# Optimization experiments

Measured on AMD Instinct MI355X. Metric: run time of the kernel, lower is better.

Reference implementation:

```python
import jax, jax.numpy as jnp
import numpy as np

H = 1024      # hidden_size
NH = 16       # attention heads
DH = H // NH  # head dim
B, S = 4, 2048
EPS = 1e-12


def setup_inputs() -> dict:
    key = jax.random.key(0)
    ks = jax.random.split(key, 9)
    sc = 1.0 / np.sqrt(H)
    inp = {
        "input_tensor": jax.random.normal(ks[0], (B, S, H), dtype=jnp.float32),
        "Wq": jax.random.normal(ks[1], (H, H), dtype=jnp.float32) * sc,
        "bq": jnp.zeros((H,), jnp.float32),
        "Wk": jax.random.normal(ks[2], (H, H), dtype=jnp.float32) * sc,
        "bk": jnp.zeros((H,), jnp.float32),
        "Wv": jax.random.normal(ks[3], (H, H), dtype=jnp.float32) * sc,
        "bv": jnp.zeros((H,), jnp.float32),
        "Wo": jax.random.normal(ks[4], (H, H), dtype=jnp.float32) * sc,
        "bo": jnp.zeros((H,), jnp.float32),
        "gamma": jnp.ones((H,), jnp.float32),
        "beta": jnp.zeros((H,), jnp.float32),
    }
    return inp


def _heads(x):
    # [B,S,H] -> [B,NH,S,DH]
    b, s, _ = x.shape
    return x.reshape(b, s, NH, DH).transpose(0, 2, 1, 3)


def reference(input_tensor, Wq, bq, Wk, bk, Wv, bv, Wo, bo, gamma, beta):
    q = _heads(input_tensor @ Wq.T + bq)
    k = _heads(input_tensor @ Wk.T + bk)
    v = _heads(input_tensor @ Wv.T + bv)
    scores = jnp.einsum("bhqd,bhkd->bhqk", q, k) / jnp.sqrt(jnp.float32(DH))
    probs = jax.nn.softmax(scores, axis=-1)  # dropout p=0 -> identity
    ctx = jnp.einsum("bhqk,bhkd->bhqd", probs, v)
    ctx = ctx.transpose(0, 2, 1, 3).reshape(input_tensor.shape)  # [B,S,H]
    h = ctx @ Wo.T + bo
    x = h + input_tensor
    u = jnp.mean(x, axis=-1, keepdims=True)
    s2 = jnp.mean((x - u) ** 2, axis=-1, keepdims=True)
    xn = (x - u) / jnp.sqrt(s2 + EPS)
    return gamma * xn + beta
```

## Files before the change

kernel.cpp:

```cpp
#include <hip/hip_runtime.h>
#include <math.h>

#define H   1024
#define NH  16
#define DH  64
#define BB  4
#define SS  2048
#define M_ROWS (BB*SS)
#define EPS 1e-12f
#define QSCALE 0.18033688011112042f

typedef __attribute__((ext_vector_type(4))) float f32x4;
typedef __attribute__((ext_vector_type(8))) short bf16x8;
typedef const __attribute__((address_space(1))) void* as1cvp;
typedef __attribute__((address_space(3))) void*       as3vp;
typedef const __attribute__((address_space(1))) ushort* as1u;
typedef __attribute__((address_space(3))) ushort*       as3u;

__device__ __forceinline__ unsigned short f2bf(float f) {
    union { float f; unsigned u; } x; x.f = f;
    unsigned r = x.u + 0x7fffu + ((x.u >> 16) & 1u);
    return (unsigned short)(r >> 16);
}
__device__ __forceinline__ unsigned pk2bf(float lo, float hi) {
    return __builtin_amdgcn_perm(__float_as_uint(hi), __float_as_uint(lo), 0x07060302u);
}

__global__ __launch_bounds__(256)
void cvt_all(const float4* __restrict__ x,
             const float4* __restrict__ wq, const float4* __restrict__ wk,
             const float4* __restrict__ wv, const float4* __restrict__ wo,
             ushort4* __restrict__ xb, ushort4* __restrict__ wqb,
             ushort4* __restrict__ wkb, ushort4* __restrict__ wvb,
             ushort4* __restrict__ wob)
{
    int id = blockIdx.x * 256 + threadIdx.x;
    const float4* src; ushort4* dst; int off;
    if (id < 2097152) { src = x; dst = xb; off = id; }
    else {
        int t = id - 2097152, wsel = t >> 18;
        off = t & 262143;
        src = wsel == 0 ? wq : wsel == 1 ? wk : wsel == 2 ? wv : wo;
        dst = wsel == 0 ? wqb : wsel == 1 ? wkb : wsel == 2 ? wvb : wob;
    }
    float4 v = src[off];
    ushort4 o; o.x = f2bf(v.x); o.y = f2bf(v.y); o.z = f2bf(v.z); o.w = f2bf(v.w);
    dst[off] = o;
}

#define GL(gsrc, ldst) __builtin_amdgcn_global_load_lds((as1cvp)(gsrc), (as3vp)(ldst), 16, 0, 0)
#define STAGE_T(ofs, kt)                                                        \
    GL(gA + aOff  + (kt) * 64,      lds + (ofs) + w512);                        \
    GL(gA + aOff  + (kt) * 64 + 32, lds + (ofs) + 4096 + w512);                 \
    GL(gB + bOff0 + (kt) * 64,      lds + (ofs) + 8192 + w1024);                \
    GL(gB + bOff0 + (kt) * 64 + 32, lds + (ofs) + 16384 + w1024);               \
    GL(gB + bOff1 + (kt) * 64,      lds + (ofs) + 8192 + w1024 + 512);          \
    GL(gB + bOff1 + (kt) * 64 + 32, lds + (ofs) + 16384 + w1024 + 512);

__device__ __forceinline__ void gemm_core_256(const ushort* __restrict__ A,
                                              const ushort* __restrict__ Wt,
                                              ushort* ldsP,
                                              int row0, int col0, int K,
                                              f32x4 (&acc)[4][4])
{
    const int tid = threadIdx.x, lane = tid & 63, w = tid >> 6;
    const int wr = w >> 2, wc = w & 3, l15 = lane & 15, quad = lane >> 4;
    const int qsw = (quad ^ ((l15 >> 1) & 3)) * 8;

    const int sc = (lane & 3) ^ ((lane >> 3) & 3);

    const as1u gA = (as1u)A;
    const as1u gB = (as1u)Wt;
    as3u lds = (as3u)ldsP;

    const size_t aOff  = (size_t)(row0 + w * 16 + (lane >> 2)) * K + sc * 8;
    const size_t bOff0 = (size_t)(col0 + w * 32 + (lane >> 2)) * K + sc * 8;
    const size_t bOff1 = (size_t)(col0 + w * 32 + 16 + (lane >> 2)) * K + sc * 8;
    const int w512 = w * 512, w1024 = w * 1024;

    const int NT = K >> 6;
    STAGE_T(0, 0);
    STAGE_T(24576, 1);

    int cur = 0;
    for (int t = 0; t < NT; ++t) {
        if (t + 1 < NT) asm volatile("s_waitcnt vmcnt(6)" ::: "memory");
        else            asm volatile("s_waitcnt vmcnt(0)" ::: "memory");
        __builtin_amdgcn_s_barrier();

        int nxt2 = cur + 49152; if (nxt2 >= 73728) nxt2 -= 73728;
        if (t + 2 < NT) { STAGE_T(nxt2, t + 2); }

        const ushort* base = ldsP + cur;
        #pragma unroll
        for (int h = 0; h < 2; ++h) {
            const ushort* Ah = base + h * 4096;
            const ushort* Bh = base + 8192 + h * 8192;
            bf16x8 af[4], bfr[4];
            #pragma unroll
            for (int rt = 0; rt < 4; ++rt)
                af[rt] = *(const bf16x8*)&Ah[(wr * 64 + rt * 16 + l15) * 32 + qsw];
            #pragma unroll
            for (int ct = 0; ct < 4; ++ct)
                bfr[ct] = *(const bf16x8*)&Bh[(wc * 64 + ct * 16 + l15) * 32 + qsw];
            #pragma unroll
            for (int rt = 0; rt < 4; ++rt)
                #pragma unroll
                for (int ct = 0; ct < 4; ++ct)
                    acc[rt][ct] = __builtin_amdgcn_mfma_f32_16x16x32_bf16(af[rt], bfr[ct], acc[rt][ct], 0, 0, 0);
        }
        cur += 24576; if (cur == 73728) cur = 0;
    }
}

__global__ __launch_bounds__(512, 2)
void qkv_gemm(const ushort* __restrict__ xb,
              const ushort* __restrict__ Wqb, const ushort* __restrict__ Wkb,
              const ushort* __restrict__ Wvb,
              const float* __restrict__ bq, const float* __restrict__ bk,
              const float* __restrict__ bv,
              ushort* __restrict__ Qb, ushort* __restrict__ Kb, ushort* __restrict__ Vt)
{
    __shared__ __align__(16) ushort Ls[3 * 24576];
    const int lin = blockIdx.x;
    const int swz = (lin & 7) * 96 + (lin >> 3);
    const int z   = swz >> 8;
    const int rem = swz & 255;
    const int row0 = (rem >> 2) * 128;
    const int col0 = (rem & 3) * 256;

    const ushort* Wt  = z == 0 ? Wqb : z == 1 ? Wkb : Wvb;
    const float* bias = z == 0 ? bq  : z == 1 ? bk  : bv;

    f32x4 acc[4][4];
    #pragma unroll
    for (int i = 0; i < 4; ++i)
        #pragma unroll
        for (int j = 0; j < 4; ++j)
            acc[i][j] = (f32x4){0.f, 0.f, 0.f, 0.f};

    gemm_core_256(xb, Wt, Ls, row0, col0, H, acc);

    const int tid = threadIdx.x, lane = tid & 63, w = tid >> 6;
    const int wr = w >> 2, wc = w & 3, l15 = lane & 15, quad = lane >> 4;

    #pragma unroll
    for (int rt = 0; rt < 4; ++rt) {
        const int r0g = row0 + wr * 64 + rt * 16 + quad * 4;
        #pragma unroll
        for (int ct = 0; ct < 4; ++ct) {
            const int c = col0 + wc * 64 + ct * 16 + l15;
            const float bs = bias[c];
            if (z == 0) {
                #pragma unroll
                for (int i = 0; i < 4; ++i)
                    Qb[(size_t)(r0g + i) * H + c] = f2bf((acc[rt][ct][i] + bs) * QSCALE);
            } else if (z == 1) {
                #pragma unroll
                for (int i = 0; i < 4; ++i)
                    Kb[(size_t)(r0g + i) * H + c] = f2bf(acc[rt][ct][i] + bs);
            } else {
                const int bb = r0g >> 11, s0 = r0g & 2047;
                const int hh = c >> 6, dd = c & 63;
                ushort4 o;
                o.x = f2bf(acc[rt][ct][0] + bs);
                o.y = f2bf(acc[rt][ct][1] + bs);
                o.z = f2bf(acc[rt][ct][2] + bs);
                o.w = f2bf(acc[rt][ct][3] + bs);
                *(ushort4*)&Vt[(((size_t)(bb * 16 + hh) * 64 + dd) << 11) + s0] = o;
            }
        }
    }
}

__global__ __launch_bounds__(512, 2)
void oproj_gemm(const ushort* __restrict__ ctxb, const ushort* __restrict__ Wob,
                const float* __restrict__ bo, const float* __restrict__ res,
                float* __restrict__ Xr)
{
    __shared__ __align__(16) ushort Ls[3 * 24576];
    const int lin = blockIdx.x;
    const int swz = (lin & 7) * 32 + (lin >> 3);
    const int row0 = (swz >> 2) * 128;
    const int col0 = (swz & 3) * 256;

    f32x4 acc[4][4];
    #pragma unroll
    for (int i = 0; i < 4; ++i)
        #pragma unroll
        for (int j = 0; j < 4; ++j)
            acc[i][j] = (f32x4){0.f, 0.f, 0.f, 0.f};

    gemm_core_256(ctxb, Wob, Ls, row0, col0, H, acc);

    const int tid = threadIdx.x, lane = tid & 63, w = tid >> 6;
    const int wr = w >> 2, wc = w & 3, l15 = lane & 15, quad = lane >> 4;

    #pragma unroll
    for (int rt = 0; rt < 4; ++rt) {
        const int r0g = row0 + wr * 64 + rt * 16 + quad * 4;
        #pragma unroll
        for (int ct = 0; ct < 4; ++ct) {
            const int c = col0 + wc * 64 + ct * 16 + l15;
            const float bs = bo[c];
            #pragma unroll
            for (int i = 0; i < 4; ++i) {
                size_t idx = (size_t)(r0g + i) * H + c;
                Xr[idx] = acc[rt][ct][i] + bs + res[idx];
            }
        }
    }
}

#define KTILE 64
#define NKT (SS / KTILE)

__global__ __launch_bounds__(256, 2)
void flash_attn_mfma(const ushort* __restrict__ Qb, const ushort* __restrict__ Kb,
                     const ushort* __restrict__ Vt, ushort* __restrict__ ctx)
{
    __shared__ __align__(16) ushort Ks[2][KTILE * 64];
    __shared__ __align__(16) ushort Vs[2][64 * KTILE];

    const int tid  = threadIdx.x;
    const int lane = tid & 63;
    const int w    = tid >> 6;
    const int l15  = lane & 15, quad = lane >> 4;
    const int bh   = blockIdx.x & 63;
    const int qt   = blockIdx.x >> 6;
    const int b    = bh >> 4, h = bh & 15;
    const int row0 = qt * 256 + w * 64;
    const size_t qk_base = (size_t)(b * SS) * H + h * DH;
    const size_t vt_base = (size_t)((b * 16 + h) * 64) * SS;

    const as1u gK = (const as1u)Kb;
    const as1u gV = (const as1u)Vt;

    const int srow = lane >> 3;
    const int c8   = lane & 7;
    const int sck0 = c8 ^ ((srow & 3) | (((w * 2 + 0) & 1) << 2));
    const int sck1 = c8 ^ ((srow & 3) | (((w * 2 + 1) & 1) << 2));

    const int fL = (l15 & 3) | (((l15 >> 2) & 1) << 2);
    const int fV = (l15 & 3) | (((l15 >> 3) & 1) << 2);
    const int rA = 8 * (l15 >> 2) + (l15 & 3);
    int kOff0[4], kOff1[4], vOff0[4], vOff1[4];
    #pragma unroll
    for (int ct = 0; ct < 4; ++ct) {
        const int r = rA + (ct & 1) * 4 + (ct >> 1) * 32;
        kOff0[ct] = r * 64 + ((quad ^ fL) * 8);
        kOff1[ct] = r * 64 + (((4 | quad) ^ fL) * 8);
    }
    #pragma unroll
    for (int dt = 0; dt < 4; ++dt) {
        const int rv = dt * 16 + l15;
        vOff0[dt] = rv * 64 + ((quad ^ fV) * 8);
        vOff1[dt] = rv * 64 + (((4 | quad) ^ fV) * 8);
    }

    bf16x8 aq[4][2];
    #pragma unroll
    for (int g = 0; g < 4; ++g) {
        const size_t qrow = qk_base + (size_t)(row0 + g * 16 + l15) * H;
        aq[g][0] = *(const bf16x8*)&Qb[qrow + quad * 8];
        aq[g][1] = *(const bf16x8*)&Qb[qrow + 32 + quad * 8];
    }

    union { unsigned u[4]; bf16x8 v; } ONES;
    #pragma unroll
    for (int i = 0; i < 4; ++i) ONES.u[i] = 0x3F803F80u;

    f32x4 acc_l[4];
    f32x4 o[4][4];
    #pragma unroll
    for (int g = 0; g < 4; ++g) {
        acc_l[g] = (f32x4){0.f, 0.f, 0.f, 0.f};
        #pragma unroll
        for (int dt = 0; dt < 4; ++dt) o[g][dt] = (f32x4){0.f, 0.f, 0.f, 0.f};
    }

    const as1u gK0 = gK + qk_base + (size_t)(w * 16 + srow) * H;
    const as1u gV0 = gV + vt_base + (size_t)(w * 16 + srow) * SS;

    __builtin_amdgcn_global_load_lds((as1cvp)(gK0 + sck0 * 8),
                                     (as3vp)(&Ks[0][(w * 16) * 64]), 16, 0, 0);
    __builtin_amdgcn_global_load_lds((as1cvp)(gK0 + (size_t)8 * H + sck1 * 8),
                                     (as3vp)(&Ks[0][(w * 16 + 8) * 64]), 16, 0, 0);
    __builtin_amdgcn_global_load_lds((as1cvp)(gV0 + sck0 * 8),
                                     (as3vp)(&Vs[0][(w * 16) * 64]), 16, 0, 0);
    __builtin_amdgcn_global_load_lds((as1cvp)(gV0 + (size_t)8 * SS + sck1 * 8),
                                     (as3vp)(&Vs[0][(w * 16 + 8) * 64]), 16, 0, 0);

    for (int kt = 0; kt < NKT; ++kt) {
        __syncthreads();

        if (kt + 1 < NKT) {
            const int j0 = (kt + 1) * KTILE;
            const int nb = (kt + 1) & 1;
            __builtin_amdgcn_global_load_lds((as1cvp)(gK0 + (size_t)j0 * H + sck0 * 8),
                                             (as3vp)(&Ks[nb][(w * 16) * 64]), 16, 0, 0);
            __builtin_amdgcn_global_load_lds((as1cvp)(gK0 + (size_t)(j0 + 8) * H + sck1 * 8),
                                             (as3vp)(&Ks[nb][(w * 16 + 8) * 64]), 16, 0, 0);
            __builtin_amdgcn_global_load_lds((as1cvp)(gV0 + j0 + sck0 * 8),
                                             (as3vp)(&Vs[nb][(w * 16) * 64]), 16, 0, 0);
            __builtin_amdgcn_global_load_lds((as1cvp)(gV0 + (size_t)8 * SS + j0 + sck1 * 8),
                                             (as3vp)(&Vs[nb][(w * 16 + 8) * 64]), 16, 0, 0);
        }

        const ushort* Ktile = Ks[kt & 1];
        const ushort* Vtile = Vs[kt & 1];

        f32x4 s[4][4];
        __builtin_amdgcn_s_setprio(1);
        #pragma unroll
        for (int ct = 0; ct < 4; ++ct) {
            const bf16x8 k0 = *(const bf16x8*)&Ktile[kOff0[ct]];
            const bf16x8 k1 = *(const bf16x8*)&Ktile[kOff1[ct]];
            #pragma unroll
            for (int g = 0; g < 4; ++g) {
                f32x4 z = (f32x4){0.f, 0.f, 0.f, 0.f};
                z = __builtin_amdgcn_mfma_f32_16x16x32_bf16(k0, aq[g][0], z, 0, 0, 0);
                z = __builtin_amdgcn_mfma_f32_16x16x32_bf16(k1, aq[g][1], z, 0, 0, 0);
                s[g][ct] = z;
            }
        }
        __builtin_amdgcn_s_setprio(0);

        union { unsigned u[4]; bf16x8 v; } A[4][2];
        #pragma unroll
        for (int g = 0; g < 4; ++g) {
            #pragma unroll
            for (int ct = 0; ct < 4; ++ct) {
                const float p0 = __builtin_amdgcn_exp2f(s[g][ct][0]);
                const float p1 = __builtin_amdgcn_exp2f(s[g][ct][1]);
                const float p2 = __builtin_amdgcn_exp2f(s[g][ct][2]);
                const float p3 = __builtin_amdgcn_exp2f(s[g][ct][3]);
                A[g][ct >> 1].u[(ct & 1) * 2 + 0] = pk2bf(p0, p1);
                A[g][ct >> 1].u[(ct & 1) * 2 + 1] = pk2bf(p2, p3);
            }
        }

        __builtin_amdgcn_s_setprio(1);
        #pragma unroll
        for (int g = 0; g < 4; ++g) {
            acc_l[g] = __builtin_amdgcn_mfma_f32_16x16x32_bf16(A[g][0].v, ONES.v, acc_l[g], 0, 0, 0);
            acc_l[g] = __builtin_amdgcn_mfma_f32_16x16x32_bf16(A[g][1].v, ONES.v, acc_l[g], 0, 0, 0);
        }
        #pragma unroll
        for (int dt = 0; dt < 4; ++dt) {
            const bf16x8 v0 = *(const bf16x8*)&Vtile[vOff0[dt]];
            const bf16x8 v1 = *(const bf16x8*)&Vtile[vOff1[dt]];
            #pragma unroll
            for (int g = 0; g < 4; ++g) {
                o[g][dt] = __builtin_amdgcn_mfma_f32_16x16x32_bf16(A[g][0].v, v0, o[g][dt], 0, 0, 0);
                o[g][dt] = __builtin_amdgcn_mfma_f32_16x16x32_bf16(A[g][1].v, v1, o[g][dt], 0, 0, 0);
            }
        }
        __builtin_amdgcn_s_setprio(0);
    }

    #pragma unroll
    for (int g = 0; g < 4; ++g) {
        #pragma unroll
        for (int i = 0; i < 4; ++i) {
            const float inv = 1.f / acc_l[g][i];
            const int r = row0 + g * 16 + quad * 4 + i;
            #pragma unroll
            for (int dt = 0; dt < 4; ++dt)
                ctx[qk_base + (size_t)r * H + dt * 16 + l15] = f2bf(o[g][dt][i] * inv);
        }
    }
}

__global__ __launch_bounds__(256)
void ln_kernel(const float* __restrict__ Xr, const float* __restrict__ gamma,
               const float* __restrict__ beta, float* __restrict__ out)
{
    __shared__ float red[4], red2[4];
    const int row = blockIdx.x;
    const int tid = threadIdx.x;
    const int lane = tid & 63, w = tid >> 6;
    const float4 v = ((const float4*)(Xr + (size_t)row * H))[tid];
    float s  = v.x + v.y + v.z + v.w;
    float ss = v.x * v.x + v.y * v.y + v.z * v.z + v.w * v.w;
    #pragma unroll
    for (int d = 1; d < 64; d <<= 1) {
        s  += __shfl_xor(s, d);
        ss += __shfl_xor(ss, d);
    }
    if (lane == 0) { red[w] = s; red2[w] = ss; }
    __syncthreads();
    s  = red[0]  + red[1]  + red[2]  + red[3];
    ss = red2[0] + red2[1] + red2[2] + red2[3];
    const float mean = s * (1.f / H);
    const float var  = ss * (1.f / H) - mean * mean;
    const float rstd = rsqrtf(var + EPS);
    const float4 g  = ((const float4*)gamma)[tid];
    const float4 be = ((const float4*)beta)[tid];
    float4 o;
    o.x = g.x * (v.x - mean) * rstd + be.x;
    o.y = g.y * (v.y - mean) * rstd + be.y;
    o.z = g.z * (v.z - mean) * rstd + be.z;
    o.w = g.w * (v.w - mean) * rstd + be.w;
    ((float4*)(out + (size_t)row * H))[tid] = o;
}

extern "C" void kernel_launch(void* const* d_in, const int* in_sizes, int n_in,
                              void* d_out, int out_size, void* d_ws, size_t ws_size,
                              hipStream_t stream)
{
    const float* x     = (const float*)d_in[0];
    const float* Wq    = (const float*)d_in[1];
    const float* bq    = (const float*)d_in[2];
    const float* Wk    = (const float*)d_in[3];
    const float* bk    = (const float*)d_in[4];
    const float* Wv    = (const float*)d_in[5];
    const float* bv    = (const float*)d_in[6];
    const float* Wo    = (const float*)d_in[7];
    const float* bo    = (const float*)d_in[8];
    const float* gamma = (const float*)d_in[9];
    const float* beta  = (const float*)d_in[10];

    char* ws = (char*)d_ws;
    ushort* xb  = (ushort*)(ws);
    ushort* Wqb = (ushort*)(ws + (size_t)(16 << 20));
    ushort* Wkb = (ushort*)(ws + (size_t)(18 << 20));
    ushort* Wvb = (ushort*)(ws + (size_t)(20 << 20));
    ushort* Wob = (ushort*)(ws + (size_t)(22 << 20));
    ushort* Qb  = (ushort*)(ws + (size_t)(24 << 20));
    ushort* Kb  = (ushort*)(ws + (size_t)(40 << 20));
    ushort* Vt  = (ushort*)(ws + (size_t)(56 << 20));
    float*  Xr  = (float*) (ws + (size_t)(40 << 20));

    cvt_all<<<12288, 256, 0, stream>>>((const float4*)x, (const float4*)Wq, (const float4*)Wk,
                                       (const float4*)Wv, (const float4*)Wo,
                                       (ushort4*)xb, (ushort4*)Wqb, (ushort4*)Wkb,
                                       (ushort4*)Wvb, (ushort4*)Wob);

    qkv_gemm<<<768, 512, 0, stream>>>(
        xb, Wqb, Wkb, Wvb, bq, bk, bv, Qb, Kb, Vt);

    flash_attn_mfma<<<BB * NH * (SS / 256), 256, 0, stream>>>(Qb, Kb, Vt, Qb );

    oproj_gemm<<<256, 512, 0, stream>>>(Qb, Wob, bo, x, Xr);

    ln_kernel<<<M_ROWS, 256, 0, stream>>>(Xr, gamma, beta, (float*)d_out);
}
```

Measured before the change: 267.7 us.

## Software-pipeline QK^T MFMAs of next row group with exp of current group

Restructures the attention inner loop so all K and V fragments are loaded from LDS up front. The QK^T MFMAs for row group g+1 are then issued before the exp2/bf16 packing and PV MFMAs of group g. This interleaves matrix-core work with VALU exponentials, aiming to hide the transcendental latency instead of running the two phases serially. It costs extra live registers for the preloaded V fragments, which could lower occupancy or cause spills.

```diff
diff --git a/kernel.cpp b/kernel.cpp
--- a/kernel.cpp
+++ b/kernel.cpp
@@ -310,50 +310,57 @@
         const ushort* Ktile = Ks[kt & 1];
         const ushort* Vtile = Vs[kt & 1];
 
-        f32x4 s[4][4];
+        bf16x8 kf0[4], kf1[4], vf0[4], vf1[4];
+        #pragma unroll
+        for (int ct = 0; ct < 4; ++ct) {
+            kf0[ct] = *(const bf16x8*)&Ktile[kOff0[ct]];
+            kf1[ct] = *(const bf16x8*)&Ktile[kOff1[ct]];
+        }
+        #pragma unroll
+        for (int dt = 0; dt < 4; ++dt) {
+            vf0[dt] = *(const bf16x8*)&Vtile[vOff0[dt]];
+            vf1[dt] = *(const bf16x8*)&Vtile[vOff1[dt]];
+        }
+
+        f32x4 sg[4][4];
         __builtin_amdgcn_s_setprio(1);
         #pragma unroll
         for (int ct = 0; ct < 4; ++ct) {
-            const bf16x8 k0 = *(const bf16x8*)&Ktile[kOff0[ct]];
-            const bf16x8 k1 = *(const bf16x8*)&Ktile[kOff1[ct]];
-            #pragma unroll
-            for (int g = 0; g < 4; ++g) {
-                f32x4 z = (f32x4){0.f, 0.f, 0.f, 0.f};
-                z = __builtin_amdgcn_mfma_f32_16x16x32_bf16(k0, aq[g][0], z, 0, 0, 0);
-                z = __builtin_amdgcn_mfma_f32_16x16x32_bf16(k1, aq[g][1], z, 0, 0, 0);
-                s[g][ct] = z;
+            f32x4 z = (f32x4){0.f, 0.f, 0.f, 0.f};
+            z = __builtin_amdgcn_mfma_f32_16x16x32_bf16(kf0[ct], aq[0][0], z, 0, 0, 0);
+            sg[0][ct] = __builtin_amdgcn_mfma_f32_16x16x32_bf16(kf1[ct], aq[0][1], z, 0, 0, 0);
+        }
+        #pragma unroll
+        for (int g = 0; g < 4; ++g) {
+            if (g + 1 < 4) {
+                #pragma unroll
+                for (int ct = 0; ct < 4; ++ct) {
+                    f32x4 z = (f32x4){0.f, 0.f, 0.f, 0.f};
+                    z = __builtin_amdgcn_mfma_f32_16x16x32_bf16(kf0[ct], aq[g + 1][0], z, 0, 0, 0);
+                    sg[g + 1][ct] = __builtin_amdgcn_mfma_f32_16x16x32_bf16(kf1[ct], aq[g + 1][1], z, 0, 0, 0);
+                }
             }
-        }
-        __builtin_amdgcn_s_setprio(0);
-
-        union { unsigned u[4]; bf16x8 v; } A[4][2];
-        #pragma unroll
-        for (int g = 0; g < 4; ++g) {
+            union { unsigned u[4]; bf16x8 v; } A0, A1;
             #pragma unroll
             for (int ct = 0; ct < 4; ++ct) {
-                const float p0 = __builtin_amdgcn_exp2f(s[g][ct][0]);
-                const float p1 = __builtin_amdgcn_exp2f(s[g][ct][1]);
-                const float p2 = __builtin_amdgcn_exp2f(s[g][ct][2]);
-                const float p3 = __builtin_amdgcn_exp2f(s[g][ct][3]);
-                A[g][ct >> 1].u[(ct & 1) * 2 + 0] = pk2bf(p0, p1);
-                A[g][ct >> 1].u[(ct & 1) * 2 + 1] = pk2bf(p2, p3);
+                const float p0 = __builtin_amdgcn_exp2f(sg[g][ct][0]);
+                const float p1 = __builtin_amdgcn_exp2f(sg[g][ct][1]);
+                const float p2 = __builtin_amdgcn_exp2f(sg[g][ct][2]);
+                const float p3 = __builtin_amdgcn_exp2f(sg[g][ct][3]);
+                if (ct < 2) {
+                    A0.u[(ct & 1) * 2 + 0] = pk2bf(p0, p1);
+                    A0.u[(ct & 1) * 2 + 1] = pk2bf(p2, p3);
+                } else {
+                    A1.u[(ct & 1) * 2 + 0] = pk2bf(p0, p1);
+                    A1.u[(ct & 1) * 2 + 1] = pk2bf(p2, p3);
+                }
             }
-        }
-
-        __builtin_amdgcn_s_setprio(1);
-        #pragma unroll
-        for (int g = 0; g < 4; ++g) {
-            acc_l[g] = __builtin_amdgcn_mfma_f32_16x16x32_bf16(A[g][0].v, ONES.v, acc_l[g], 0, 0, 0);
-            acc_l[g] = __builtin_amdgcn_mfma_f32_16x16x32_bf16(A[g][1].v, ONES.v, acc_l[g], 0, 0, 0);
-        }
-        #pragma unroll
-        for (int dt = 0; dt < 4; ++dt) {
-            const bf16x8 v0 = *(const bf16x8*)&Vtile[vOff0[dt]];
-            const bf16x8 v1 = *(const bf16x8*)&Vtile[vOff1[dt]];
-            #pragma unroll
-            for (int g = 0; g < 4; ++g) {
-                o[g][dt] = __builtin_amdgcn_mfma_f32_16x16x32_bf16(A[g][0].v, v0, o[g][dt], 0, 0, 0);
-                o[g][dt] = __builtin_amdgcn_mfma_f32_16x16x32_bf16(A[g][1].v, v1, o[g][dt], 0, 0, 0);
+            acc_l[g] = __builtin_amdgcn_mfma_f32_16x16x32_bf16(A0.v, ONES.v, acc_l[g], 0, 0, 0);
+            acc_l[g] = __builtin_amdgcn_mfma_f32_16x16x32_bf16(A1.v, ONES.v, acc_l[g], 0, 0, 0);
+            #pragma unroll
+            for (int dt = 0; dt < 4; ++dt) {
+                o[g][dt] = __builtin_amdgcn_mfma_f32_16x16x32_bf16(A0.v, vf0[dt], o[g][dt], 0, 0, 0);
+                o[g][dt] = __builtin_amdgcn_mfma_f32_16x16x32_bf16(A1.v, vf1[dt], o[g][dt], 0, 0, 0);
             }
         }
         __builtin_amdgcn_s_setprio(0);
```

Result: no change. 265.7 us (-0.7%).
